# Optimization experiments

Hardware: AMD Instinct MI355X
Metric: run time of the kernel (lower is better)

The kernel has to match this reference:

```python
import jax, jax.numpy as jnp
import numpy as np

B, H, S, D = 4, 8, 2048, 64
NEG = -1e9


def setup_inputs() -> dict:
    key = jax.random.key(0)
    k1, k2, k3, k4 = jax.random.split(key, 4)
    qs = jax.random.normal(k1, (B, H, S, D), dtype=jnp.float32)
    ks = jax.random.normal(k2, (B, H, S, D), dtype=jnp.float32)
    vs = jax.random.normal(k3, (B, H, S, D), dtype=jnp.float32)
    # binary 0/1 float mask, broadcast over heads
    mask = (jax.random.uniform(k4, (B, 1, S, S)) < 0.5).astype(jnp.float32)
    return {"qs": qs, "ks": ks, "vs": vs, "mask": mask}


def reference(qs, ks, vs, mask):
    scale = 1.0 / np.sqrt(qs.shape[-1]).astype(np.float32)
    # [B,H,S,S] logits; multiplicative pre-mask, then additive -1e9 on masked slots
    logits = jnp.einsum('bhqd,bhkd->bhqk', qs, ks) * mask * scale
    logits = logits + (1.0 - mask) * NEG
    weights = jax.nn.softmax(logits, axis=-1) * mask  # multiplicative post-mask
    return jnp.einsum('bhqk,bhkd->bhqd', weights, vs)
```

## Files before the change

kernel.cpp:

```cpp
#include <hip/hip_runtime.h>
#include <stdint.h>

#define S_LEN 2048
#define NTILE 32

typedef float f32x4 __attribute__((ext_vector_type(4)));
typedef float f32x16 __attribute__((ext_vector_type(16)));
typedef short bf16x8 __attribute__((ext_vector_type(8)));

__device__ __forceinline__ uint16_t f2bf(float f) {
    uint32_t u = __float_as_uint(f);
    return (uint16_t)((u + 0x7FFFu + ((u >> 16) & 1u)) >> 16);
}

#define AS3PTR(p) ((__attribute__((address_space(3))) uint32_t*)(uintptr_t)(p))
#define AS1PTR(p) ((const __attribute__((address_space(1))) uint32_t*)(uintptr_t)(p))

__global__ __launch_bounds__(256)
void prep_all(const float* __restrict__ K, const float* __restrict__ V,
              const float* __restrict__ M, uint8_t* __restrict__ Kd,
              uint8_t* __restrict__ Vd, uint16_t* __restrict__ Mp)
{
    __shared__ float mt[4096];
    const int bid = blockIdx.x;
    const int tid = threadIdx.x;
    if (bid < 2048) {
        int flat = bid * 256 + tid;
        int s = flat & 511, tile = flat >> 9;
        int key = s >> 3, dc = (s >> 1) & 3, h = s & 1;
        int kt = tile & 31, bh = tile >> 5;
        const float* src = K + (((size_t)bh * S_LEN + kt * 64 + key) << 6) + dc * 16 + h * 8;
        f32x4 a = *(const f32x4*)src;
        f32x4 b = *(const f32x4*)(src + 4);
        bf16x8 o;
        o[0] = (short)f2bf(a[0]); o[1] = (short)f2bf(a[1]);
        o[2] = (short)f2bf(a[2]); o[3] = (short)f2bf(a[3]);
        o[4] = (short)f2bf(b[0]); o[5] = (short)f2bf(b[1]);
        o[6] = (short)f2bf(b[2]); o[7] = (short)f2bf(b[3]);
        *(bf16x8*)(Kd + ((size_t)tile << 13) + (((dc * 2 + h) * 64 + key) << 4)) = o;
    } else if (bid < 4096) {
        int flat = (bid - 2048) * 256 + tid;
        int s = flat & 511, tile = flat >> 9;
        int d = s & 63, h = (s >> 6) & 1, ku = s >> 7;
        int kt = tile & 31, bh = tile >> 5;
        const float* src = V + (((size_t)bh * S_LEN + kt * 64 + ku * 16 + h * 8) << 6) + d;
        bf16x8 o;
        #pragma unroll
        for (int j = 0; j < 8; ++j) o[j] = (short)f2bf(src[j << 6]);
        *(bf16x8*)(Vd + ((size_t)tile << 13) + (((ku * 2 + h) * 64 + d) << 4)) = o;
    } else {
        int mid = bid - 4096;
        int b = mid >> 10, qt = (mid >> 5) & 31, kt = mid & 31;
        int row = tid >> 2, cc = tid & 3;
        const float* src = M + ((size_t)(b * S_LEN + qt * 64 + row) * S_LEN) + kt * 64;
        #pragma unroll
        for (int i = 0; i < 4; ++i)
            *(f32x4*)&mt[(row << 6) + cc * 16 + i * 4] =
                *(const f32x4*)(src + cc * 16 + i * 4);
        __syncthreads();
        int l = tid & 63, w = tid >> 6;
        int qw = w >> 1, kw = w & 1, h = l >> 5, l31 = l & 31;
        uint32_t m = 0;
        #pragma unroll
        for (int r = 0; r < 16; ++r) {
            int keyl = 32 * kw + (r & 3) + 8 * (r >> 2) + 4 * h;
            m |= (mt[((32 * qw + l31) << 6) + keyl] > 0.5f) << r;
        }
        Mp[((size_t)mid << 8) + tid] = (uint16_t)m;
    }
}

__global__ __launch_bounds__(256, 4)
void attn_fwd(const float* __restrict__ Q, const uint8_t* __restrict__ Kd,
              const uint8_t* __restrict__ Vd, const uint16_t* __restrict__ Mp,
              float* __restrict__ O)
{
    __shared__ __align__(16) uint8_t lds[32768];

    const int tid  = threadIdx.x;
    const int lane = tid & 63;
    const int w    = tid >> 6;
    const int qw   = w >> 1;
    const int kw   = w & 1;
    const int h    = lane >> 5;
    const int l31  = lane & 31;

    const int bid0 = blockIdx.x;
    const int bid  = ((bid0 & 7) << 7) + (bid0 >> 3);
    const int bh  = bid >> 5;
    const int qt  = bid & 31;
    const int b   = bh >> 3;
    const int q0  = qt << 6;

    const float QSCL = 0.125f * 1.44269504088896340736f;
    bf16x8 qf[4];
    {
        const float* qrow = Q + (((size_t)bh * S_LEN + q0 + 32 * qw + l31) << 6);
        #pragma unroll
        for (int dc = 0; dc < 4; ++dc) {
            f32x4 a  = *(const f32x4*)(qrow + dc * 16 + h * 8);
            f32x4 b4 = *(const f32x4*)(qrow + dc * 16 + h * 8 + 4);
            bf16x8 f;
            f[0] = (short)f2bf(a[0] * QSCL);  f[1] = (short)f2bf(a[1] * QSCL);
            f[2] = (short)f2bf(a[2] * QSCL);  f[3] = (short)f2bf(a[3] * QSCL);
            f[4] = (short)f2bf(b4[0] * QSCL); f[5] = (short)f2bf(b4[1] * QSCL);
            f[6] = (short)f2bf(b4[2] * QSCL); f[7] = (short)f2bf(b4[3] * QSCL);
            qf[dc] = f;
        }
    }

    f32x16 acc[2];
    acc[0] = (f32x16)(0.f);
    acc[1] = (f32x16)(0.f);
    float lsum = 0.f;

    const uint8_t*  kst = Kd + (((size_t)bh * 32) << 13) + (w << 10) + lane * 16;
    const uint8_t*  vst = Vd + (((size_t)bh * 32) << 13) + (w << 10) + lane * 16;
    const uint16_t* mst = Mp + (((size_t)(b * 32 + qt) * 32) << 8) + (w << 6) + lane;

    uint32_t mreg[2];
    f32x16 sA, sB;

#define STAGE_K(T, SLOT)                                                        \
    {                                                                           \
        size_t toff = (size_t)(T) << 13;                                        \
        __builtin_amdgcn_global_load_lds(AS1PTR(kst + toff),                    \
            AS3PTR(&lds[(SLOT) * 8192 + (w << 10)]), 16, 0, 0);                 \
        __builtin_amdgcn_global_load_lds(AS1PTR(kst + toff + 4096),             \
            AS3PTR(&lds[(SLOT) * 8192 + 4096 + (w << 10)]), 16, 0, 0);          \
    }
#define STAGE_V(T, SLOT)                                                        \
    {                                                                           \
        size_t toff = (size_t)(T) << 13;                                        \
        __builtin_amdgcn_global_load_lds(AS1PTR(vst + toff),                    \
            AS3PTR(&lds[16384 + (SLOT) * 8192 + (w << 10)]), 16, 0, 0);         \
        __builtin_amdgcn_global_load_lds(AS1PTR(vst + toff + 4096),             \
            AS3PTR(&lds[16384 + (SLOT) * 8192 + 4096 + (w << 10)]), 16, 0, 0);  \
    }
#define LOADM(T, R)  mreg[R] = mst[(size_t)(T) << 8];

#define QK(SREG, PAR)                                                           \
    {                                                                           \
        const uint8_t* kb = &lds[(PAR) * 8192];                                 \
        SREG = (f32x16)(0.f);                                                   \
        __builtin_amdgcn_s_setprio(1);                                          \
        _Pragma("unroll")                                                       \
        for (int dc = 0; dc < 4; ++dc) {                                        \
            bf16x8 kf = *(const bf16x8*)(kb + (((dc * 2 + h) * 64 + 32 * kw + l31) << 4)); \
            SREG = __builtin_amdgcn_mfma_f32_32x32x16_bf16(kf, qf[dc], SREG, 0, 0, 0); \
        }                                                                       \
        __builtin_amdgcn_s_setprio(0);                                          \
    }

#define SMPV(SREG, PAR, MR)                                                     \
    {                                                                           \
        uint32_t mw = mreg[MR];                                                 \
        uint32_t pd[8];                                                         \
        _Pragma("unroll")                                                       \
        for (int rq = 0; rq < 8; ++rq) {                                        \
            float e0, e1;                                                       \
            asm("v_exp_f32 %0, %1" : "=v"(e0) : "v"(SREG[2 * rq]));             \
            asm("v_exp_f32 %0, %1" : "=v"(e1) : "v"(SREG[2 * rq + 1]));         \
            int32_t m0 = ((int32_t)(mw << (31 - 2 * rq))) >> 31;                \
            int32_t m1 = ((int32_t)(mw << (30 - 2 * rq))) >> 31;                \
            float p0 = __int_as_float(__float_as_int(e0) & m0);                 \
            float p1 = __int_as_float(__float_as_int(e1) & m1);                 \
            lsum += p0; lsum += p1;                                             \
            asm("v_cvt_pk_bf16_f32 %0, %1, %2" : "=v"(pd[rq]) : "v"(p0), "v"(p1)); \
        }                                                                       \
        _Pragma("unroll")                                                       \
        for (int u = 0; u < 2; ++u) {                                           \
            asm("v_permlane32_swap_b32 %0, %1" : "+v"(pd[4*u]),   "+v"(pd[4*u+2])); \
            asm("v_permlane32_swap_b32 %0, %1" : "+v"(pd[4*u+1]), "+v"(pd[4*u+3])); \
        }                                                                       \
        const uint8_t* vbuf = &lds[16384 + (PAR) * 8192];                       \
        __builtin_amdgcn_s_setprio(1);                                          \
        _Pragma("unroll")                                                       \
        for (int u = 0; u < 2; ++u) {                                           \
            union { uint32_t d[4]; bf16x8 v; } pa;                              \
            pa.d[0] = pd[4*u]; pa.d[1] = pd[4*u+1];                             \
            pa.d[2] = pd[4*u+2]; pa.d[3] = pd[4*u+3];                           \
            _Pragma("unroll")                                                   \
            for (int dblk = 0; dblk < 2; ++dblk) {                              \
                bf16x8 vf = *(const bf16x8*)(vbuf +                             \
                    ((((kw * 2 + u) * 2 + h) * 64 + 32 * dblk + l31) << 4));    \
                acc[dblk] = __builtin_amdgcn_mfma_f32_32x32x16_bf16(pa.v, vf, acc[dblk], 0, 0, 0); \
            }                                                                   \
        }                                                                       \
        __builtin_amdgcn_s_setprio(0);                                          \
    }

#define SYNC(N)                                                                 \
    asm volatile("s_waitcnt vmcnt(" #N ")" ::: "memory");                       \
    __builtin_amdgcn_s_barrier();                                               \
    __builtin_amdgcn_sched_barrier(0);

#define BODY(T, SP, SN, PAR, DOK)                                               \
    {                                                                           \
        SYNC(0);                                                                \
        STAGE_V((T) + 1, (PAR) ^ 1);                                            \
        if (DOK) STAGE_K((T) + 2, PAR);                                         \
        LOADM((T) + 1, (PAR) ^ 1);                                              \
        QK(SN, (PAR) ^ 1);                                                      \
        SMPV(SP, PAR, PAR);                                                     \
    }

    STAGE_K(0, 0);
    STAGE_V(0, 0);
    STAGE_K(1, 1);
    LOADM(0, 0);
    asm volatile("s_waitcnt vmcnt(5)" ::: "memory");
    __builtin_amdgcn_s_barrier();
    __builtin_amdgcn_sched_barrier(0);
    QK(sA, 0);

    #pragma unroll 1
    for (int i = 0; i < 15; ++i) {
        int t = i * 2;
        BODY(t,     sA, sB, 0, true);
        BODY(t + 1, sB, sA, 1, true);
    }
    BODY(30, sA, sB, 0, false);
    SYNC(0);
    SMPV(sB, 1, 1);

#undef BODY
#undef SYNC
#undef SMPV
#undef QK
#undef LOADM
#undef STAGE_V
#undef STAGE_K

    lsum += __shfl_xor(lsum, 32, 64);

    __syncthreads();
    float* ex  = (float*)lds;
    float* ex2 = (float*)(lds + 16384);
    if (kw == 1) {
        #pragma unroll
        for (int dblk = 0; dblk < 2; ++dblk)
            #pragma unroll
            for (int rq = 0; rq < 4; ++rq) {
                f32x4 v = { acc[dblk][4 * rq], acc[dblk][4 * rq + 1],
                            acc[dblk][4 * rq + 2], acc[dblk][4 * rq + 3] };
                *(f32x4*)&ex[(qw << 11) + (((dblk << 2) + rq) << 8) + (lane << 2)] = v;
            }
        if (lane < 32) ex2[(qw << 5) + lane] = lsum;
    }
    __syncthreads();
    if (kw == 0) {
        #pragma unroll
        for (int dblk = 0; dblk < 2; ++dblk)
            #pragma unroll
            for (int rq = 0; rq < 4; ++rq) {
                f32x4 v = *(const f32x4*)&ex[(qw << 11) + (((dblk << 2) + rq) << 8) + (lane << 2)];
                acc[dblk][4 * rq]     += v[0];
                acc[dblk][4 * rq + 1] += v[1];
                acc[dblk][4 * rq + 2] += v[2];
                acc[dblk][4 * rq + 3] += v[3];
            }
        float l = lsum + ex2[(qw << 5) + l31];
        float linv = (l > 0.f) ? 1.f / l : 0.f;

        float* obase = O + (((size_t)bh * S_LEN + q0 + 32 * qw) << 6);
        #pragma unroll
        for (int r = 0; r < 16; ++r) {
            int qloc = (r & 3) + 8 * (r >> 2) + 4 * h;
            float inv = __shfl(linv, qloc, 64);
            obase[(qloc << 6) + l31]      = acc[0][r] * inv;
            obase[(qloc << 6) + 32 + l31] = acc[1][r] * inv;
        }
    }
}

extern "C" void kernel_launch(void* const* d_in, const int* in_sizes, int n_in,
                              void* d_out, int out_size, void* d_ws, size_t ws_size,
                              hipStream_t stream) {
    const float* qs   = (const float*)d_in[0];
    const float* ks   = (const float*)d_in[1];
    const float* vs   = (const float*)d_in[2];
    const float* mask = (const float*)d_in[3];
    float* out = (float*)d_out;
    (void)in_sizes; (void)n_in; (void)out_size; (void)ws_size;

    uint8_t* ws = (uint8_t*)d_ws;
    uint8_t* Kd = ws;
    uint8_t* Vd = ws + (8u << 20);
    uint16_t* Mp = (uint16_t*)(ws + (16u << 20));

    hipLaunchKernelGGL(prep_all, dim3(8192), dim3(256), 0, stream,
                       ks, vs, mask, Kd, Vd, Mp);
    hipLaunchKernelGGL(attn_fwd, dim3(1024), dim3(256), 0, stream,
                       qs, Kd, Vd, Mp, out);
}
```

Measured before the change: 80.82 us.

## Interleave QK and PV MFMAs and hoist LDS fragment loads per iteration

Restructures the loop body so that all K and V fragments are read from LDS up front, and the next tile's QK MFMAs are interleaved with the current tile's PV MFMAs. This breaks the serial dependency chain on a single accumulator and gives the matrix pipe independent work while the softmax exp runs. It also precomputes per-lane LDS offsets, replaces the shift-based mask extraction with v_bfe_i32, and keeps the row sum as a two-lane vector accumulator. The prologue wait is tightened to vmcnt(0), which may add a little startup latency. More fragments live at once, which raises register pressure.

New measurement: 104.1 us. 28.8% more time.

```diff
diff --git a/kernel.cpp b/kernel.cpp
--- a/kernel.cpp
+++ b/kernel.cpp
@@ -4,6 +4,7 @@
 #define S_LEN 2048
 #define NTILE 32
 
+typedef float f32x2 __attribute__((ext_vector_type(2)));
 typedef float f32x4 __attribute__((ext_vector_type(4)));
 typedef float f32x16 __attribute__((ext_vector_type(16)));
 typedef short bf16x8 __attribute__((ext_vector_type(8)));
@@ -112,60 +113,57 @@
     f32x16 acc[2];
     acc[0] = (f32x16)(0.f);
     acc[1] = (f32x16)(0.f);
-    float lsum = 0.f;
-
-    const uint8_t*  kst = Kd + (((size_t)bh * 32) << 13) + (w << 10) + lane * 16;
-    const uint8_t*  vst = Vd + (((size_t)bh * 32) << 13) + (w << 10) + lane * 16;
-    const uint16_t* mst = Mp + (((size_t)(b * 32 + qt) * 32) << 8) + (w << 6) + lane;
+    f32x2 lsum2 = (f32x2){0.f, 0.f};
+
+    const uint8_t*  kbh_u = Kd + (((size_t)bh * 32) << 13);
+    const uint8_t*  vbh_u = Vd + (((size_t)bh * 32) << 13);
+    const uint16_t* mst   = Mp + (((size_t)(b * 32 + qt) * 32) << 8) + (w << 6) + lane;
+    const int vgl = (w << 10) + lane * 16;
+
+    const int lane_k = (h << 10) + (kw << 9) + (l31 << 4);
+    const int lane_v = (kw << 12) + (h << 10) + (l31 << 4);
 
     uint32_t mreg[2];
     f32x16 sA, sB;
 
 #define STAGE_K(T, SLOT)                                                        \
     {                                                                           \
-        size_t toff = (size_t)(T) << 13;                                        \
-        __builtin_amdgcn_global_load_lds(AS1PTR(kst + toff),                    \
+        const uint8_t* kt_u = kbh_u + ((size_t)(T) << 13);                      \
+        __builtin_amdgcn_global_load_lds(AS1PTR(kt_u + vgl),                    \
             AS3PTR(&lds[(SLOT) * 8192 + (w << 10)]), 16, 0, 0);                 \
-        __builtin_amdgcn_global_load_lds(AS1PTR(kst + toff + 4096),             \
+        __builtin_amdgcn_global_load_lds(AS1PTR(kt_u + 4096 + vgl),             \
             AS3PTR(&lds[(SLOT) * 8192 + 4096 + (w << 10)]), 16, 0, 0);          \
     }
 #define STAGE_V(T, SLOT)                                                        \
     {                                                                           \
-        size_t toff = (size_t)(T) << 13;                                        \
-        __builtin_amdgcn_global_load_lds(AS1PTR(vst + toff),                    \
+        const uint8_t* vt_u = vbh_u + ((size_t)(T) << 13);                      \
+        __builtin_amdgcn_global_load_lds(AS1PTR(vt_u + vgl),                    \
             AS3PTR(&lds[16384 + (SLOT) * 8192 + (w << 10)]), 16, 0, 0);         \
-        __builtin_amdgcn_global_load_lds(AS1PTR(vst + toff + 4096),             \
+        __builtin_amdgcn_global_load_lds(AS1PTR(vt_u + 4096 + vgl),             \
             AS3PTR(&lds[16384 + (SLOT) * 8192 + 4096 + (w << 10)]), 16, 0, 0);  \
     }
 #define LOADM(T, R)  mreg[R] = mst[(size_t)(T) << 8];
 
-#define QK(SREG, PAR)                                                           \
-    {                                                                           \
-        const uint8_t* kb = &lds[(PAR) * 8192];                                 \
-        SREG = (f32x16)(0.f);                                                   \
-        __builtin_amdgcn_s_setprio(1);                                          \
-        _Pragma("unroll")                                                       \
-        for (int dc = 0; dc < 4; ++dc) {                                        \
-            bf16x8 kf = *(const bf16x8*)(kb + (((dc * 2 + h) * 64 + 32 * kw + l31) << 4)); \
-            SREG = __builtin_amdgcn_mfma_f32_32x32x16_bf16(kf, qf[dc], SREG, 0, 0, 0); \
-        }                                                                       \
-        __builtin_amdgcn_s_setprio(0);                                          \
-    }
-
-#define SMPV(SREG, PAR, MR)                                                     \
+#define SYNC(N)                                                                 \
+    asm volatile("s_waitcnt vmcnt(" #N ")" ::: "memory");                       \
+    __builtin_amdgcn_s_barrier();                                               \
+    __builtin_amdgcn_sched_barrier(0);
+
+#define SM(SREG, MR)                                                            \
+    uint32_t pd[8];                                                             \
     {                                                                           \
         uint32_t mw = mreg[MR];                                                 \
-        uint32_t pd[8];                                                         \
         _Pragma("unroll")                                                       \
         for (int rq = 0; rq < 8; ++rq) {                                        \
             float e0, e1;                                                       \
             asm("v_exp_f32 %0, %1" : "=v"(e0) : "v"(SREG[2 * rq]));             \
             asm("v_exp_f32 %0, %1" : "=v"(e1) : "v"(SREG[2 * rq + 1]));         \
-            int32_t m0 = ((int32_t)(mw << (31 - 2 * rq))) >> 31;                \
-            int32_t m1 = ((int32_t)(mw << (30 - 2 * rq))) >> 31;                \
+            int m0, m1;                                                         \
+            asm("v_bfe_i32 %0, %1, %2, 1" : "=v"(m0) : "v"(mw), "i"(2 * rq));   \
+            asm("v_bfe_i32 %0, %1, %2, 1" : "=v"(m1) : "v"(mw), "i"(2 * rq + 1)); \
             float p0 = __int_as_float(__float_as_int(e0) & m0);                 \
             float p1 = __int_as_float(__float_as_int(e1) & m1);                 \
-            lsum += p0; lsum += p1;                                             \
+            lsum2 += (f32x2){p0, p1};                                           \
             asm("v_cvt_pk_bf16_f32 %0, %1, %2" : "=v"(pd[rq]) : "v"(p0), "v"(p1)); \
         }                                                                       \
         _Pragma("unroll")                                                       \
@@ -173,27 +171,7 @@
             asm("v_permlane32_swap_b32 %0, %1" : "+v"(pd[4*u]),   "+v"(pd[4*u+2])); \
             asm("v_permlane32_swap_b32 %0, %1" : "+v"(pd[4*u+1]), "+v"(pd[4*u+3])); \
         }                                                                       \
-        const uint8_t* vbuf = &lds[16384 + (PAR) * 8192];                       \
-        __builtin_amdgcn_s_setprio(1);                                          \
-        _Pragma("unroll")                                                       \
-        for (int u = 0; u < 2; ++u) {                                           \
-            union { uint32_t d[4]; bf16x8 v; } pa;                              \
-            pa.d[0] = pd[4*u]; pa.d[1] = pd[4*u+1];                             \
-            pa.d[2] = pd[4*u+2]; pa.d[3] = pd[4*u+3];                           \
-            _Pragma("unroll")                                                   \
-            for (int dblk = 0; dblk < 2; ++dblk) {                              \
-                bf16x8 vf = *(const bf16x8*)(vbuf +                             \
-                    ((((kw * 2 + u) * 2 + h) * 64 + 32 * dblk + l31) << 4));    \
-                acc[dblk] = __builtin_amdgcn_mfma_f32_32x32x16_bf16(pa.v, vf, acc[dblk], 0, 0, 0); \
-            }                                                                   \
-        }                                                                       \
-        __builtin_amdgcn_s_setprio(0);                                          \
-    }
-
-#define SYNC(N)                                                                 \
-    asm volatile("s_waitcnt vmcnt(" #N ")" ::: "memory");                       \
-    __builtin_amdgcn_s_barrier();                                               \
-    __builtin_amdgcn_sched_barrier(0);
+    }
 
 #define BODY(T, SP, SN, PAR, DOK)                                               \
     {                                                                           \
@@ -201,18 +179,51 @@
         STAGE_V((T) + 1, (PAR) ^ 1);                                            \
         if (DOK) STAGE_K((T) + 2, PAR);                                         \
         LOADM((T) + 1, (PAR) ^ 1);                                              \
-        QK(SN, (PAR) ^ 1);                                                      \
-        SMPV(SP, PAR, PAR);                                                     \
+                     \
+        const uint8_t* kbp = &lds[((PAR) ^ 1) * 8192] + lane_k;                 \
+        const uint8_t* vbp = &lds[16384 + (PAR) * 8192] + lane_v;               \
+        bf16x8 kf0 = *(const bf16x8*)(kbp);                                     \
+        bf16x8 kf1 = *(const bf16x8*)(kbp + 2048);                              \
+        bf16x8 kf2 = *(const bf16x8*)(kbp + 4096);                              \
+        bf16x8 kf3 = *(const bf16x8*)(kbp + 6144);                              \
+        bf16x8 vf0 = *(const bf16x8*)(vbp);                                     \
+        bf16x8 vf1 = *(const bf16x8*)(vbp + 512);                               \
+        bf16x8 vf2 = *(const bf16x8*)(vbp + 2048);                              \
+        bf16x8 vf3 = *(const bf16x8*)(vbp + 2560);                              \
+        SM(SP, PAR);                                                            \
+        union { uint32_t d[4]; bf16x8 v; } pa0, pa1;                            \
+        pa0.d[0] = pd[0]; pa0.d[1] = pd[1]; pa0.d[2] = pd[2]; pa0.d[3] = pd[3]; \
+        pa1.d[0] = pd[4]; pa1.d[1] = pd[5]; pa1.d[2] = pd[6]; pa1.d[3] = pd[7]; \
+        __builtin_amdgcn_s_setprio(1);                                          \
+        SN = __builtin_amdgcn_mfma_f32_32x32x16_bf16(kf0, qf[0], (f32x16)(0.f), 0, 0, 0); \
+        acc[0] = __builtin_amdgcn_mfma_f32_32x32x16_bf16(pa0.v, vf0, acc[0], 0, 0, 0);    \
+        acc[1] = __builtin_amdgcn_mfma_f32_32x32x16_bf16(pa0.v, vf1, acc[1], 0, 0, 0);    \
+        SN = __builtin_amdgcn_mfma_f32_32x32x16_bf16(kf1, qf[1], SN, 0, 0, 0);  \
+        acc[0] = __builtin_amdgcn_mfma_f32_32x32x16_bf16(pa1.v, vf2, acc[0], 0, 0, 0);    \
+        SN = __builtin_amdgcn_mfma_f32_32x32x16_bf16(kf2, qf[2], SN, 0, 0, 0);  \
+        acc[1] = __builtin_amdgcn_mfma_f32_32x32x16_bf16(pa1.v, vf3, acc[1], 0, 0, 0);    \
+        SN = __builtin_amdgcn_mfma_f32_32x32x16_bf16(kf3, qf[3], SN, 0, 0, 0);  \
+        __builtin_amdgcn_s_setprio(0);                                          \
     }
 
     STAGE_K(0, 0);
     STAGE_V(0, 0);
     STAGE_K(1, 1);
     LOADM(0, 0);
-    asm volatile("s_waitcnt vmcnt(5)" ::: "memory");
-    __builtin_amdgcn_s_barrier();
-    __builtin_amdgcn_sched_barrier(0);
-    QK(sA, 0);
+    SYNC(0);
+    {
+        const uint8_t* kbp = &lds[0] + lane_k;
+        bf16x8 kf0 = *(const bf16x8*)(kbp);
+        bf16x8 kf1 = *(const bf16x8*)(kbp + 2048);
+        bf16x8 kf2 = *(const bf16x8*)(kbp + 4096);
+        bf16x8 kf3 = *(const bf16x8*)(kbp + 6144);
+        __builtin_amdgcn_s_setprio(1);
+        sA = __builtin_amdgcn_mfma_f32_32x32x16_bf16(kf0, qf[0], (f32x16)(0.f), 0, 0, 0);
+        sA = __builtin_amdgcn_mfma_f32_32x32x16_bf16(kf1, qf[1], sA, 0, 0, 0);
+        sA = __builtin_amdgcn_mfma_f32_32x32x16_bf16(kf2, qf[2], sA, 0, 0, 0);
+        sA = __builtin_amdgcn_mfma_f32_32x32x16_bf16(kf3, qf[3], sA, 0, 0, 0);
+        __builtin_amdgcn_s_setprio(0);
+    }
 
     #pragma unroll 1
     for (int i = 0; i < 15; ++i) {
@@ -221,17 +232,34 @@
         BODY(t + 1, sB, sA, 1, true);
     }
     BODY(30, sA, sB, 0, false);
-    SYNC(0);
-    SMPV(sB, 1, 1);
+
+    {
+        SYNC(0);
+        const uint8_t* vbp = &lds[16384 + 8192] + lane_v;
+        bf16x8 vf0 = *(const bf16x8*)(vbp);
+        bf16x8 vf1 = *(const bf16x8*)(vbp + 512);
+        bf16x8 vf2 = *(const bf16x8*)(vbp + 2048);
+        bf16x8 vf3 = *(const bf16x8*)(vbp + 2560);
+        SM(sB, 1);
+        union { uint32_t d[4]; bf16x8 v; } pa0, pa1;
+        pa0.d[0] = pd[0]; pa0.d[1] = pd[1]; pa0.d[2] = pd[2]; pa0.d[3] = pd[3];
+        pa1.d[0] = pd[4]; pa1.d[1] = pd[5]; pa1.d[2] = pd[6]; pa1.d[3] = pd[7];
+        __builtin_amdgcn_s_setprio(1);
+        acc[0] = __builtin_amdgcn_mfma_f32_32x32x16_bf16(pa0.v, vf0, acc[0], 0, 0, 0);
+        acc[1] = __builtin_amdgcn_mfma_f32_32x32x16_bf16(pa0.v, vf1, acc[1], 0, 0, 0);
+        acc[0] = __builtin_amdgcn_mfma_f32_32x32x16_bf16(pa1.v, vf2, acc[0], 0, 0, 0);
+        acc[1] = __builtin_amdgcn_mfma_f32_32x32x16_bf16(pa1.v, vf3, acc[1], 0, 0, 0);
+        __builtin_amdgcn_s_setprio(0);
+    }
 
 #undef BODY
+#undef SM
 #undef SYNC
-#undef SMPV
-#undef QK
 #undef LOADM
 #undef STAGE_V
 #undef STAGE_K
 
+    float lsum = lsum2[0] + lsum2[1];
     lsum += __shfl_xor(lsum, 32, 64);
 
     __syncthreads();
```
